# Kernel optimization log

Hardware: AMD Instinct MI355X
Metric: run time of the kernel (lower is better)

Reference implementation:

```python
import jax, jax.numpy as jnp
import numpy as np

H = 64
L = 4
SCALE = 1.0 / np.sqrt(H)  # PyTorch default init bound


def _gru_dir(x, wih, whh, bi, bh, reverse):
    # x: (T, B, D_in); returns (final_h (B,H), outputs (T,B,H))
    xs = x[::-1] if reverse else x
    h0 = jnp.zeros((x.shape[1], H), x.dtype)

    def step(h, xt):
        gi = xt @ wih.T + bi            # (B, 3H)
        gh = h @ whh.T + bh             # (B, 3H)
        ir, iz, inn = jnp.split(gi, 3, axis=-1)
        hr, hz, hn = jnp.split(gh, 3, axis=-1)
        r = jax.nn.sigmoid(ir + hr)
        z = jax.nn.sigmoid(iz + hz)
        n = jnp.tanh(inn + r * hn)
        h_new = (1.0 - z) * n + z * h
        return h_new, h_new

    hT, ys = jax.lax.scan(step, h0, xs)
    if reverse:
        ys = ys[::-1]
    return hT, ys


def setup_inputs() -> dict:
    key = jax.random.key(0)
    ks = jax.random.split(key, 6)
    u = lambda k, shape: jax.random.uniform(k, shape, jnp.float32, -SCALE, SCALE)
    return {
        "mfcc": jax.random.normal(ks[0], (1024, 256, 64), jnp.float32),
        "Wih0": u(ks[1], (2, 3 * H, H)),          # layer 0, 2 directions, input dim 64
        "Wih": u(ks[2], (3, 2, 3 * H, 2 * H)),    # layers 1-3, input dim 128 (bidir)
        "Whh": u(ks[3], (L, 2, 3 * H, H)),
        "bih": u(ks[4], (L, 2, 3 * H)),
        "bhh": u(ks[5], (L, 2, 3 * H)),
    }


def reference(mfcc, Wih0, Wih, Whh, bih, bhh):
    x = mfcc
    finals = []  # flat index layer*2 + direction, matching PyTorch h_n layout
    for l in range(L):
        outs = []
        for d in range(2):
            wih = Wih0[d] if l == 0 else Wih[l - 1, d]
            hT, ys = _gru_dir(x, wih, Whh[l, d], bih[l, d], bhh[l, d], reverse=(d == 1))
            finals.append(hT)
            outs.append(ys)
        x = jnp.concatenate(outs, axis=-1)  # (T, B, 2H)
    # Original: cat(hidden[NUM_HIDDEN-1], hidden[NUM_HIDDEN << 1-1]) == cat(hidden[3], hidden[4])
    return jnp.concatenate((finals[3], finals[4]), axis=1)  # (B, 2H)
```

## Files before the change

### kernel.cpp

```cpp
#include <hip/hip_runtime.h>
#include <cstddef>
#include <cstdint>

#define T_SEQ 1024
#define BATCH 256
#define HID   64
#define G3    192
#define CHK   128
#define NCHK  (T_SEQ / CHK)

typedef unsigned short ushort_t;

__device__ __forceinline__ float sigm_f(float x) {
    return __fdividef(1.f, 1.f + __expf(-x));
}
__device__ __forceinline__ float tanh_f(float x) {
    return 1.f - __fdividef(2.f, 1.f + __expf(2.f * x));
}
__device__ __forceinline__ ushort_t f2bf_rne(float f) {
    uint32_t u = __float_as_uint(f);
    uint32_t r = (u + 0x7FFFu + ((u >> 16) & 1u)) >> 16;
    return (ushort_t)r;
}
__device__ __forceinline__ float bf2f(ushort_t u) {
    return __uint_as_float(((uint32_t)u) << 16);
}

__device__ __forceinline__ float4 load4f(const float* p) { return *(const float4*)p; }
__device__ __forceinline__ float4 load4f(const ushort_t* p) {
    ushort4 u = *(const ushort4*)p;
    float4 f;
    f.x = bf2f(u.x); f.y = bf2f(u.y); f.z = bf2f(u.z); f.w = bf2f(u.w);
    return f;
}

template<typename TX, int K>
__global__ __launch_bounds__(256) void gi_gemm_chunk(
    const TX* __restrict__ x,
    const float* __restrict__ w,
    long w_dir_stride,
    const float* __restrict__ bias,
    long bias_dir_stride,
    float* __restrict__ gi,
    int c)
{
    __shared__ float xs[64][65];
    __shared__ float wsm[64][65];

    const int tid = threadIdx.x;
    const int mb  = blockIdx.x;
    const int nb  = blockIdx.y;
    const int d   = blockIdx.z;

    const int t_local = mb >> 2;
    const int boff    = (mb & 3) * 64;
    const int t_glob  = d ? (T_SEQ - 1 - c * CHK - t_local) : (c * CHK + t_local);

    const TX*    xg = x + ((size_t)t_glob * BATCH + boff) * K;
    const float* wg = w + (size_t)d * w_dir_stride + (size_t)nb * 64 * K;
    float* op = gi + ((size_t)d * CHK * BATCH + (size_t)t_local * BATCH + boff) * G3 + nb * 64;

    const int r0 = (tid >> 4) << 2;
    const int c0 = (tid & 15) << 2;
    float acc[4][4] = {};

    for (int kc = 0; kc < K; kc += 64) {
        #pragma unroll
        for (int i = 0; i < 4; ++i) {
            int ch  = tid + i * 256;
            int row = ch >> 4;
            int col = (ch & 15) << 2;
            float4 v = load4f(xg + (size_t)row * K + kc + col);
            xs[row][col+0] = v.x; xs[row][col+1] = v.y;
            xs[row][col+2] = v.z; xs[row][col+3] = v.w;
            float4 u = load4f(wg + (size_t)row * K + kc + col);
            wsm[row][col+0] = u.x; wsm[row][col+1] = u.y;
            wsm[row][col+2] = u.z; wsm[row][col+3] = u.w;
        }
        __syncthreads();
        #pragma unroll 8
        for (int k = 0; k < 64; ++k) {
            float a0 = xs[r0+0][k], a1 = xs[r0+1][k], a2 = xs[r0+2][k], a3 = xs[r0+3][k];
            float b0 = wsm[c0+0][k], b1 = wsm[c0+1][k], b2 = wsm[c0+2][k], b3 = wsm[c0+3][k];
            acc[0][0] = fmaf(a0,b0,acc[0][0]); acc[0][1] = fmaf(a0,b1,acc[0][1]);
            acc[0][2] = fmaf(a0,b2,acc[0][2]); acc[0][3] = fmaf(a0,b3,acc[0][3]);
            acc[1][0] = fmaf(a1,b0,acc[1][0]); acc[1][1] = fmaf(a1,b1,acc[1][1]);
            acc[1][2] = fmaf(a1,b2,acc[1][2]); acc[1][3] = fmaf(a1,b3,acc[1][3]);
            acc[2][0] = fmaf(a2,b0,acc[2][0]); acc[2][1] = fmaf(a2,b1,acc[2][1]);
            acc[2][2] = fmaf(a2,b2,acc[2][2]); acc[2][3] = fmaf(a2,b3,acc[2][3]);
            acc[3][0] = fmaf(a3,b0,acc[3][0]); acc[3][1] = fmaf(a3,b1,acc[3][1]);
            acc[3][2] = fmaf(a3,b2,acc[3][2]); acc[3][3] = fmaf(a3,b3,acc[3][3]);
        }
        __syncthreads();
    }

    const float* bp = bias + (size_t)d * bias_dir_stride + nb * 64;
    float4 bv = *(const float4*)(bp + c0);
    #pragma unroll
    for (int i = 0; i < 4; ++i) {
        float4 o;
        o.x = acc[i][0] + bv.x; o.y = acc[i][1] + bv.y;
        o.z = acc[i][2] + bv.z; o.w = acc[i][3] + bv.w;
        *(float4*)(op + (size_t)(r0 + i) * G3 + c0) = o;
    }
}

__global__ __launch_bounds__(64) void gru_recur_chunk(
    const float* __restrict__ gi,
    const float* __restrict__ WhhL,
    const float* __restrict__ bhhL,
    ushort_t* __restrict__ ys,
    float* __restrict__ hbuf,
    float* __restrict__ fin,
    int fin_dir,
    int c)
{
    const int b = blockIdx.x;
    const int d = blockIdx.y;
    const int j = threadIdx.x;

    const float* W = WhhL + (size_t)d * G3 * HID;
    float wr[HID], wz[HID], wn[HID];
    #pragma unroll
    for (int q = 0; q < HID / 4; ++q) {
        float4 a = *(const float4*)(W + (size_t)j * HID + 4*q);
        wr[4*q+0] = a.x; wr[4*q+1] = a.y; wr[4*q+2] = a.z; wr[4*q+3] = a.w;
        float4 bq = *(const float4*)(W + (size_t)(HID + j) * HID + 4*q);
        wz[4*q+0] = bq.x; wz[4*q+1] = bq.y; wz[4*q+2] = bq.z; wz[4*q+3] = bq.w;
        float4 cq = *(const float4*)(W + (size_t)(2*HID + j) * HID + 4*q);
        wn[4*q+0] = cq.x; wn[4*q+1] = cq.y; wn[4*q+2] = cq.z; wn[4*q+3] = cq.w;
    }
    const float* bh = bhhL + (size_t)d * G3;
    const float bhr = bh[j], bhz = bh[HID + j], bhn = bh[2*HID + j];

    const float* gib = gi + (size_t)d * CHK * BATCH * G3;

    float h = (c == 0) ? 0.f : hbuf[((size_t)d * BATCH + b) * HID + j];

    auto gaddr = [&](int i) -> const float* {
        return gib + ((size_t)i * BATCH + b) * G3;
    };

    const float* p = gaddr(0);
    float grA = p[j], gzA = p[HID + j], gnA = p[2*HID + j];
    p = gaddr(1);
    float grB = p[j], gzB = p[HID + j], gnB = p[2*HID + j];

    auto step = [&](float gr, float gz, float gn, int i_) {
        float accr = bhr, accz = bhz, accn = bhn;
        #pragma unroll
        for (int k = 0; k < HID; ++k) {
            float hk = __int_as_float(__builtin_amdgcn_readlane(__float_as_int(h), k));
            accr = fmaf(hk, wr[k], accr);
            accz = fmaf(hk, wz[k], accz);
            accn = fmaf(hk, wn[k], accn);
        }
        float r = sigm_f(gr + accr);
        float z = sigm_f(gz + accz);
        float n = tanh_f(gn + r * accn);
        h = (1.f - z) * n + z * h;
        if (ys != nullptr) {
            int tg = d ? (T_SEQ - 1 - c * CHK - i_) : (c * CHK + i_);
            ys[((size_t)tg * BATCH + b) * (2 * HID) + d * HID + j] = f2bf_rne(h);
        }
    };

    for (int i = 0; i < CHK; i += 2) {
        step(grA, gzA, gnA, i);
        if (i + 2 < CHK) { p = gaddr(i + 2); grA = p[j]; gzA = p[HID+j]; gnA = p[2*HID+j]; }
        step(grB, gzB, gnB, i + 1);
        if (i + 3 < CHK) { p = gaddr(i + 3); grB = p[j]; gzB = p[HID+j]; gnB = p[2*HID+j]; }
    }

    hbuf[((size_t)d * BATCH + b) * HID + j] = h;

    if (fin != nullptr && d == fin_dir) {
        fin[(size_t)b * 128 + j] = h;
    }
}

extern "C" void kernel_launch(void* const* d_in, const int* in_sizes, int n_in,
                              void* d_out, int out_size, void* d_ws, size_t ws_size,
                              hipStream_t stream) {
    (void)in_sizes; (void)n_in; (void)out_size; (void)ws_size;

    const float* mfcc = (const float*)d_in[0];
    const float* Wih0 = (const float*)d_in[1];
    const float* Wih  = (const float*)d_in[2];
    const float* Whh  = (const float*)d_in[3];
    const float* bih  = (const float*)d_in[4];
    const float* bhh  = (const float*)d_in[5];
    float* out = (float*)d_out;

    char* p = (char*)d_ws;
    ushort_t* ysA = (ushort_t*)p;  p += (size_t)T_SEQ * BATCH * 128 * 2;
    ushort_t* ysB = (ushort_t*)p;  p += (size_t)T_SEQ * BATCH * 128 * 2;
    float*    gi  = (float*)p;     p += (size_t)2 * CHK * BATCH * G3 * 4;
    float*    hb  = (float*)p;

    const dim3 ggrid2(CHK * BATCH / 64, 3, 2);
    const dim3 ggrid1(CHK * BATCH / 64, 3, 1);

    for (int c = 0; c < NCHK; ++c) {
        gi_gemm_chunk<float, 64><<<ggrid2, 256, 0, stream>>>(
            mfcc, Wih0, (long)G3 * HID, bih, G3, gi, c);
        gru_recur_chunk<<<dim3(BATCH, 2), 64, 0, stream>>>(
            gi, Whh, bhh, ysA, hb, nullptr, -1, c);
    }

    for (int c = 0; c < NCHK; ++c) {
        gi_gemm_chunk<ushort_t, 128><<<ggrid2, 256, 0, stream>>>(
            ysA, Wih, (long)G3 * 2 * HID, bih + 2 * G3, G3, gi, c);
        gru_recur_chunk<<<dim3(BATCH, 2), 64, 0, stream>>>(
            gi, Whh + 2 * (size_t)G3 * HID, bhh + 2 * G3, ysB, hb,
            (c == NCHK - 1) ? out : nullptr, 1, c);
    }

    for (int c = 0; c < NCHK; ++c) {
        gi_gemm_chunk<ushort_t, 128><<<ggrid1, 256, 0, stream>>>(
            ysB, Wih + 2 * (size_t)G3 * 2 * HID, 0, bih + 4 * G3, 0, gi, c);
        gru_recur_chunk<<<dim3(BATCH, 1), 64, 0, stream>>>(
            gi, Whh + 4 * (size_t)G3 * HID, bhh + 4 * G3, nullptr, hb,
            (c == NCHK - 1) ? (out + HID) : nullptr, 0, c);
    }
}
```

Measured before the change: 3.757 ms.

## Split GRU recurrent matvec across four waves with LDS partial-sum reduction

The recurrent kernel now runs 256 threads per batch row instead of 64. Each of the four waves holds a 16-wide K-slice of Whh and computes partial r/z/n dot products. The partials are combined through double-buffered shared memory with one barrier per step. This shortens the serial dependent-FMA and readlane chain per timestep and cuts register pressure from the 192 weight registers. In exchange it adds an LDS round trip and a block barrier to every step, and all waves repeat the gate math while only wave 0 stores.

```diff
diff --git a/kernel.cpp b/kernel.cpp
--- a/kernel.cpp
+++ b/kernel.cpp
@@ -8,6 +8,7 @@
 #define G3    192
 #define CHK   128
 #define NCHK  (T_SEQ / CHK)
+#define KSLC  16
 
 typedef unsigned short ushort_t;
 
@@ -105,7 +106,7 @@
     }
 }
 
-__global__ __launch_bounds__(64) void gru_recur_chunk(
+__global__ __launch_bounds__(256) void gru_recur_chunk(
     const float* __restrict__ gi,
     const float* __restrict__ WhhL,
     const float* __restrict__ bhhL,
@@ -115,19 +116,24 @@
     int fin_dir,
     int c)
 {
+    __shared__ float pr[2][4][64];
+    __shared__ float pz[2][4][64];
+    __shared__ float pn[2][4][64];
+
     const int b = blockIdx.x;
     const int d = blockIdx.y;
-    const int j = threadIdx.x;
+    const int j = threadIdx.x & 63;
+    const int w = __builtin_amdgcn_readfirstlane(threadIdx.x >> 6);
 
     const float* W = WhhL + (size_t)d * G3 * HID;
-    float wr[HID], wz[HID], wn[HID];
+    float wr[KSLC], wz[KSLC], wn[KSLC];
     #pragma unroll
-    for (int q = 0; q < HID / 4; ++q) {
-        float4 a = *(const float4*)(W + (size_t)j * HID + 4*q);
+    for (int q = 0; q < KSLC / 4; ++q) {
+        float4 a = *(const float4*)(W + (size_t)j * HID + w * KSLC + 4*q);
         wr[4*q+0] = a.x; wr[4*q+1] = a.y; wr[4*q+2] = a.z; wr[4*q+3] = a.w;
-        float4 bq = *(const float4*)(W + (size_t)(HID + j) * HID + 4*q);
+        float4 bq = *(const float4*)(W + (size_t)(HID + j) * HID + w * KSLC + 4*q);
         wz[4*q+0] = bq.x; wz[4*q+1] = bq.y; wz[4*q+2] = bq.z; wz[4*q+3] = bq.w;
-        float4 cq = *(const float4*)(W + (size_t)(2*HID + j) * HID + 4*q);
+        float4 cq = *(const float4*)(W + (size_t)(2*HID + j) * HID + w * KSLC + 4*q);
         wn[4*q+0] = cq.x; wn[4*q+1] = cq.y; wn[4*q+2] = cq.z; wn[4*q+3] = cq.w;
     }
     const float* bh = bhhL + (size_t)d * G3;
@@ -146,36 +152,47 @@
     p = gaddr(1);
     float grB = p[j], gzB = p[HID + j], gnB = p[2*HID + j];
 
-    auto step = [&](float gr, float gz, float gn, int i_) {
-        float accr = bhr, accz = bhz, accn = bhn;
+    const bool store_wave = (w == 0);
+
+    auto step = [&](float gr, float gz, float gn, int i_, int par) {
+        float ar = 0.f, az = 0.f, an = 0.f;
         #pragma unroll
-        for (int k = 0; k < HID; ++k) {
-            float hk = __int_as_float(__builtin_amdgcn_readlane(__float_as_int(h), k));
-            accr = fmaf(hk, wr[k], accr);
-            accz = fmaf(hk, wz[k], accz);
-            accn = fmaf(hk, wn[k], accn);
-        }
+        for (int kk = 0; kk < KSLC; ++kk) {
+            float hk = __int_as_float(
+                __builtin_amdgcn_readlane(__float_as_int(h), w * KSLC + kk));
+            ar = fmaf(hk, wr[kk], ar);
+            az = fmaf(hk, wz[kk], az);
+            an = fmaf(hk, wn[kk], an);
+        }
+        pr[par][w][j] = ar;
+        pz[par][w][j] = az;
+        pn[par][w][j] = an;
+        __syncthreads();
+        float accr = bhr + ((pr[par][0][j] + pr[par][1][j]) + (pr[par][2][j] + pr[par][3][j]));
+        float accz = bhz + ((pz[par][0][j] + pz[par][1][j]) + (pz[par][2][j] + pz[par][3][j]));
+        float accn = bhn + ((pn[par][0][j] + pn[par][1][j]) + (pn[par][2][j] + pn[par][3][j]));
         float r = sigm_f(gr + accr);
         float z = sigm_f(gz + accz);
         float n = tanh_f(gn + r * accn);
         h = (1.f - z) * n + z * h;
-        if (ys != nullptr) {
+        if (store_wave && ys != nullptr) {
             int tg = d ? (T_SEQ - 1 - c * CHK - i_) : (c * CHK + i_);
             ys[((size_t)tg * BATCH + b) * (2 * HID) + d * HID + j] = f2bf_rne(h);
         }
     };
 
     for (int i = 0; i < CHK; i += 2) {
-        step(grA, gzA, gnA, i);
+        step(grA, gzA, gnA, i, 0);
         if (i + 2 < CHK) { p = gaddr(i + 2); grA = p[j]; gzA = p[HID+j]; gnA = p[2*HID+j]; }
-        step(grB, gzB, gnB, i + 1);
+        step(grB, gzB, gnB, i + 1, 1);
         if (i + 3 < CHK) { p = gaddr(i + 3); grB = p[j]; gzB = p[HID+j]; gnB = p[2*HID+j]; }
     }
 
-    hbuf[((size_t)d * BATCH + b) * HID + j] = h;
-
-    if (fin != nullptr && d == fin_dir) {
-        fin[(size_t)b * 128 + j] = h;
+    if (store_wave) {
+        hbuf[((size_t)d * BATCH + b) * HID + j] = h;
+        if (fin != nullptr && d == fin_dir) {
+            fin[(size_t)b * 128 + j] = h;
+        }
     }
 }
 
@@ -204,14 +221,14 @@
     for (int c = 0; c < NCHK; ++c) {
         gi_gemm_chunk<float, 64><<<ggrid2, 256, 0, stream>>>(
             mfcc, Wih0, (long)G3 * HID, bih, G3, gi, c);
-        gru_recur_chunk<<<dim3(BATCH, 2), 64, 0, stream>>>(
+        gru_recur_chunk<<<dim3(BATCH, 2), 256, 0, stream>>>(
             gi, Whh, bhh, ysA, hb, nullptr, -1, c);
     }
 
     for (int c = 0; c < NCHK; ++c) {
         gi_gemm_chunk<ushort_t, 128><<<ggrid2, 256, 0, stream>>>(
             ysA, Wih, (long)G3 * 2 * HID, bih + 2 * G3, G3, gi, c);
-        gru_recur_chunk<<<dim3(BATCH, 2), 64, 0, stream>>>(
+        gru_recur_chunk<<<dim3(BATCH, 2), 256, 0, stream>>>(
             gi, Whh + 2 * (size_t)G3 * HID, bhh + 2 * G3, ysB, hb,
             (c == NCHK - 1) ? out : nullptr, 1, c);
     }
@@ -219,7 +236,7 @@
     for (int c = 0; c < NCHK; ++c) {
         gi_gemm_chunk<ushort_t, 128><<<ggrid1, 256, 0, stream>>>(
             ysB, Wih + 2 * (size_t)G3 * 2 * HID, 0, bih + 4 * G3, 0, gi, c);
-        gru_recur_chunk<<<dim3(BATCH, 1), 64, 0, stream>>>(
+        gru_recur_chunk<<<dim3(BATCH, 1), 256, 0, stream>>>(
             gi, Whh + 4 * (size_t)G3 * HID, bhh + 4 * G3, nullptr, hb,
             (c == NCHK - 1) ? (out + HID) : nullptr, 0, c);
     }
```

Result: faster. 3.139 ms (-16.5%).
